# Kernel tuning notes

Hardware: AMD Instinct MI355X
Metric: run time of the kernel (lower is better)

The kernel has to match this reference:

```python
import jax, jax.numpy as jnp
import numpy as np

B, T, C, H = 4, 2048, 1024, 16
DH = C // H  # 64


def setup_inputs() -> dict:
    key = jax.random.key(0)
    k_x, k_qkv, k_proj = jax.random.split(key, 3)
    x = jax.random.normal(k_x, (B, T, C), dtype=jnp.float32)
    # variance-scaling (fan_in) init for linear weights, torch layout [out, in]
    qkv_w = jax.random.normal(k_qkv, (3 * C, C), dtype=jnp.float32) * (1.0 / np.sqrt(C))
    qkv_b = jnp.zeros((3 * C,), dtype=jnp.float32)
    proj_w = jax.random.normal(k_proj, (C, C), dtype=jnp.float32) * (1.0 / np.sqrt(C))
    proj_b = jnp.zeros((C,), dtype=jnp.float32)
    # causal mask, broadcastable to [B, H, T, T]
    mask = jnp.tril(jnp.ones((T, T), dtype=bool))[None, None]
    return {"x": x, "qkv_w": qkv_w, "qkv_b": qkv_b,
            "proj_w": proj_w, "proj_b": proj_b, "mask": mask}


def reference(x, qkv_w, qkv_b, proj_w, proj_b, mask):
    b, t, c = x.shape
    scale = DH ** -0.5
    qkv = (x @ qkv_w.T + qkv_b).reshape(b, t, 3, H, DH)
    qkv = jnp.transpose(qkv, (2, 0, 3, 1, 4))  # [3, B, H, T, DH]
    q, k, v = qkv[0], qkv[1], qkv[2]
    attn = jnp.einsum("bhqd,bhkd->bhqk", q, k) * scale  # [B, H, T, T]
    neg = -jnp.finfo(attn.dtype).max
    attn = jnp.where(mask, attn, neg)
    attn = jax.nn.softmax(attn, axis=-1)
    out = jnp.einsum("bhqk,bhkd->bhqd", attn, v)  # [B, H, T, DH]
    out = jnp.transpose(out, (0, 2, 1, 3)).reshape(b, t, c)
    return out @ proj_w.T + proj_b
```

## Files before the change

kernel.cpp:

```cpp
#include <hip/hip_runtime.h>
#include <hip/hip_bf16.h>
#include <stdint.h>

#define B_ 4
#define T_ 2048
#define C_ 1024
#define H_ 16
#define DH_ 64
#define M_ (B_*T_)
#define NQKV_ (3*C_)
#define K_ C_

typedef __attribute__((ext_vector_type(8))) short short8;
typedef __attribute__((ext_vector_type(4))) float f32x4;
typedef __attribute__((ext_vector_type(4))) unsigned short us4;

union BFC { __hip_bfloat16 h; unsigned short u; };
__device__ inline unsigned short f2b(float f){ BFC c; c.h = __float2bfloat16(f); return c.u; }

__device__ inline void gload_lds16(const void* g, void* l){
  __builtin_amdgcn_global_load_lds(
    (const __attribute__((address_space(1))) void*)(uintptr_t)g,
    (__attribute__((address_space(3))) void*)(uintptr_t)l,
    16, 0, 0);
}

__global__ void cvt_f32_bf16(const float* __restrict__ src,
                             __hip_bfloat16* __restrict__ dst, int n4)
{
  int i = blockIdx.x * blockDim.x + threadIdx.x;
  int stride = gridDim.x * blockDim.x;
  for (; i < n4; i += stride) {
    float4 v = reinterpret_cast<const float4*>(src)[i];
    us4 o;
    o.x = f2b(v.x); o.y = f2b(v.y); o.z = f2b(v.z); o.w = f2b(v.w);
    reinterpret_cast<us4*>(dst)[i] = o;
  }
}

__global__ __launch_bounds__(256) void gemm_bt(
    const __hip_bfloat16* __restrict__ A,
    const __hip_bfloat16* __restrict__ Bw,
    const float* __restrict__ bias,
    int mode,
    __hip_bfloat16* __restrict__ qdst,
    __hip_bfloat16* __restrict__ kdst,
    __hip_bfloat16* __restrict__ vdst,
    float* __restrict__ fdst)
{
  __shared__ char a_lds[8192];
  __shared__ char b_lds[8192];

  const int tid = threadIdx.x;
  const int lane = tid & 63;
  const int w = tid >> 6;
  const int l15 = lane & 15;
  const int lhi = lane >> 4;
  const int wm = w >> 1, wn = w & 1;
  const int row0 = blockIdx.y * 128;
  const int col0 = blockIdx.x * 128;

  int srow[2], scol[2];
#pragma unroll
  for (int j = 0; j < 2; ++j) {
    int L = w * 2048 + j * 1024 + lane * 16;
    int r = L >> 6;
    int cb = (L & 63) ^ (((r >> 1) & 3) << 4);
    srow[j] = r;
    scol[j] = cb >> 1;
  }

  const f32x4 zf = {0.f, 0.f, 0.f, 0.f};
  f32x4 acc[4][4];
#pragma unroll
  for (int m = 0; m < 4; ++m)
#pragma unroll
    for (int n = 0; n < 4; ++n) acc[m][n] = zf;

  const short* Ag = (const short*)A;
  const short* Bg = (const short*)Bw;

  for (int kt = 0; kt < K_; kt += 32) {
    gload_lds16(Ag + (size_t)(row0 + srow[0]) * K_ + kt + scol[0], a_lds + w * 2048);
    gload_lds16(Ag + (size_t)(row0 + srow[1]) * K_ + kt + scol[1], a_lds + w * 2048 + 1024);
    gload_lds16(Bg + (size_t)(col0 + srow[0]) * K_ + kt + scol[0], b_lds + w * 2048);
    gload_lds16(Bg + (size_t)(col0 + srow[1]) * K_ + kt + scol[1], b_lds + w * 2048 + 1024);
    __syncthreads();

    short8 af[4], bfr[4];
#pragma unroll
    for (int m = 0; m < 4; ++m) {
      int r = wm * 64 + m * 16 + l15;
      af[m] = *(const short8*)(a_lds + r * 64 + ((lhi * 16) ^ (((r >> 1) & 3) << 4)));
    }
#pragma unroll
    for (int n = 0; n < 4; ++n) {
      int r = wn * 64 + n * 16 + l15;
      bfr[n] = *(const short8*)(b_lds + r * 64 + ((lhi * 16) ^ (((r >> 1) & 3) << 4)));
    }
#pragma unroll
    for (int m = 0; m < 4; ++m)
#pragma unroll
      for (int n = 0; n < 4; ++n)
        acc[m][n] = __builtin_amdgcn_mfma_f32_16x16x32_bf16(af[m], bfr[n], acc[m][n], 0, 0, 0);
    __syncthreads();
  }

  if (mode == 0) {
#pragma unroll
    for (int m = 0; m < 4; ++m) {
#pragma unroll
      for (int r = 0; r < 4; ++r) {
        int grow = row0 + wm * 64 + m * 16 + lhi * 4 + r;
        int b = grow >> 11, tt = grow & 2047;
#pragma unroll
        for (int n = 0; n < 4; ++n) {
          int gcol = col0 + wn * 64 + n * 16 + l15;
          float v = acc[m][n][r] + bias[gcol];
          int sel = gcol >> 10;
          int c1 = gcol & 1023;
          int hh = c1 >> 6, dh = c1 & 63;
          __hip_bfloat16 bv = __float2bfloat16(v);
          if (sel == 0)
            qdst[(((size_t)(b * H_ + hh)) * T_ + tt) * DH_ + dh] = bv;
          else if (sel == 1)
            kdst[(((size_t)(b * H_ + hh)) * T_ + tt) * DH_ + dh] = bv;
          else
            vdst[(((size_t)(b * H_ + hh)) * DH_ + dh) * T_ + tt] = bv;
        }
      }
    }
  } else {
#pragma unroll
    for (int m = 0; m < 4; ++m) {
#pragma unroll
      for (int r = 0; r < 4; ++r) {
        int grow = row0 + wm * 64 + m * 16 + lhi * 4 + r;
#pragma unroll
        for (int n = 0; n < 4; ++n) {
          int gcol = col0 + wn * 64 + n * 16 + l15;
          fdst[(size_t)grow * C_ + gcol] = acc[m][n][r] + bias[gcol];
        }
      }
    }
  }
}

__global__ __launch_bounds__(512, 2) void attn_kernel(
    const __hip_bfloat16* __restrict__ qg,
    const __hip_bfloat16* __restrict__ kg,
    const __hip_bfloat16* __restrict__ vtg,
    __hip_bfloat16* __restrict__ og)
{
  __shared__ char k_lds[2][8192];
  __shared__ char v_lds[2][8192];
  __shared__ char p_lds[8][4096];

  const int tid = threadIdx.x;
  const int lane = tid & 63;
  const int w = tid >> 6;
  const int l15 = lane & 15;
  const int lhi = lane >> 4;
  const int blk = blockIdx.x;
  const int bh = blk & 63;
  const int g = blk >> 6;
  const int qb = (g < 4) ? g : 11 - g;
  const int qr0 = qb * 256 + w * 32;
  const int nt = 4 * (qb + 1);
  const int tmask = qr0 >> 6;

  const char* kpb = (const char*)(kg + (size_t)bh * T_ * DH_);
  const char* vtpb = (const char*)(vtg + (size_t)bh * DH_ * T_);
  const short* qp = (const short*)(qg + (size_t)bh * T_ * DH_);
  char* pwl = p_lds[w];

  const int srow = tid >> 3;
  const int scb = ((tid & 7) << 4) ^ ((srow & 7) << 4);
  const int sdst = tid * 16;

  short8 qf[2][2];
#pragma unroll
  for (int m = 0; m < 2; ++m)
#pragma unroll
    for (int kf = 0; kf < 2; ++kf)
      qf[m][kf] = *(const short8*)(qp + (size_t)(qr0 + m * 16 + l15) * DH_ +
                                   kf * 32 + lhi * 8);

  const f32x4 zf = {0.f, 0.f, 0.f, 0.f};
  f32x4 o[2][4];
  float lsum[2][4];
#pragma unroll
  for (int m = 0; m < 2; ++m) {
#pragma unroll
    for (int n = 0; n < 4; ++n) o[m][n] = zf;
#pragma unroll
    for (int r = 0; r < 4; ++r) lsum[m][r] = 0.f;
  }

  gload_lds16(kpb + (size_t)srow * 128 + scb, &k_lds[0][sdst]);
  gload_lds16(vtpb + (size_t)srow * 4096 + scb, &v_lds[0][sdst]);
  __syncthreads();

  for (int t = 0; t < nt; ++t) {
    const int cur = t & 1;
    if (t + 1 < nt) {
      const int kv1 = (t + 1) * 64;
      gload_lds16(kpb + (size_t)(kv1 + srow) * 128 + scb, &k_lds[cur ^ 1][sdst]);
      gload_lds16(vtpb + (size_t)srow * 4096 + kv1 * 2 + scb, &v_lds[cur ^ 1][sdst]);
    }

    if (t <= tmask) {
      const int kv0 = t * 64;

      short8 kfr[2][4];
#pragma unroll
      for (int kf = 0; kf < 2; ++kf)
#pragma unroll
        for (int n = 0; n < 4; ++n) {
          int kr = n * 16 + l15;
          kfr[kf][n] = *(const short8*)(&k_lds[cur][kr * 128 +
                           ((kf * 64 + lhi * 16) ^ ((kr & 7) << 4))]);
        }

      f32x4 s[2][4];
#pragma unroll
      for (int m = 0; m < 2; ++m)
#pragma unroll
        for (int n = 0; n < 4; ++n) s[m][n] = zf;
#pragma unroll
      for (int kf = 0; kf < 2; ++kf)
#pragma unroll
        for (int n = 0; n < 4; ++n)
#pragma unroll
          for (int m = 0; m < 2; ++m)
            s[m][n] = __builtin_amdgcn_mfma_f32_16x16x32_bf16(qf[m][kf], kfr[kf][n],
                                                              s[m][n], 0, 0, 0);

      short8 vfr[2][4];
#pragma unroll
      for (int kf = 0; kf < 2; ++kf)
#pragma unroll
        for (int n = 0; n < 4; ++n) {
          int vr = n * 16 + l15;
          vfr[kf][n] = *(const short8*)(&v_lds[cur][vr * 128 +
                           ((kf * 64 + lhi * 16) ^ ((vr & 7) << 4))]);
        }

      if (t == tmask) {
#pragma unroll
        for (int m = 0; m < 2; ++m)
#pragma unroll
          for (int n = 0; n < 4; ++n)
#pragma unroll
            for (int r = 0; r < 4; ++r) {
              int kvA = kv0 + n * 16 + l15;
              int qA = qr0 + m * 16 + lhi * 4 + r;
              if (kvA > qA) s[m][n][r] = -1e30f;
            }
      }

#pragma unroll
      for (int m = 0; m < 2; ++m)
#pragma unroll
        for (int n = 0; n < 4; ++n)
#pragma unroll
          for (int r = 0; r < 4; ++r) {
            float pe = __expf(s[m][n][r] * 0.125f);
            s[m][n][r] = pe;
            lsum[m][r] += pe;
          }

#pragma unroll
      for (int m = 0; m < 2; ++m)
#pragma unroll
        for (int n = 0; n < 4; ++n)
#pragma unroll
          for (int r = 0; r < 4; ++r) {
            int row = m * 16 + lhi * 4 + r;
            *(unsigned short*)(pwl + row * 128 +
                               (((n * 16 + l15) * 2) ^ ((row & 7) << 4))) =
                f2b(s[m][n][r]);
          }
      short8 pa[2][2];
#pragma unroll
      for (int m = 0; m < 2; ++m)
#pragma unroll
        for (int kf = 0; kf < 2; ++kf) {
          int row = m * 16 + l15;
          pa[m][kf] = *(const short8*)(pwl + row * 128 +
                                       ((kf * 64 + lhi * 16) ^ ((row & 7) << 4)));
        }

#pragma unroll
      for (int kf = 0; kf < 2; ++kf)
#pragma unroll
        for (int n = 0; n < 4; ++n)
#pragma unroll
          for (int m = 0; m < 2; ++m)
            o[m][n] = __builtin_amdgcn_mfma_f32_16x16x32_bf16(pa[m][kf], vfr[kf][n],
                                                              o[m][n], 0, 0, 0);
    }

    __syncthreads();
  }

#pragma unroll
  for (int m = 0; m < 2; ++m)
#pragma unroll
    for (int r = 0; r < 4; ++r)
#pragma unroll
      for (int d = 1; d < 16; d <<= 1)
        lsum[m][r] += __shfl_xor(lsum[m][r], d, 64);

  const int b = bh >> 4, hd = bh & 15;
#pragma unroll
  for (int m = 0; m < 2; ++m)
#pragma unroll
    for (int r = 0; r < 4; ++r) {
      float inv = 1.f / lsum[m][r];
      int qrow = qr0 + m * 16 + lhi * 4 + r;
      __hip_bfloat16* orow = og + ((size_t)(b * T_ + qrow)) * C_ + hd * DH_;
#pragma unroll
      for (int n = 0; n < 4; ++n)
        orow[n * 16 + l15] = __float2bfloat16(o[m][n][r] * inv);
    }
}

extern "C" void kernel_launch(void* const* d_in, const int* in_sizes, int n_in,
                              void* d_out, int out_size, void* d_ws, size_t ws_size,
                              hipStream_t stream) {
  const float* x      = (const float*)d_in[0];
  const float* qkv_w  = (const float*)d_in[1];
  const float* qkv_b  = (const float*)d_in[2];
  const float* proj_w = (const float*)d_in[3];
  const float* proj_b = (const float*)d_in[4];
  float* out = (float*)d_out;

  char* ws = (char*)d_ws;
  __hip_bfloat16* xb    = (__hip_bfloat16*)(ws);
  __hip_bfloat16* wqkv  = (__hip_bfloat16*)(ws + 16777216);
  __hip_bfloat16* wproj = (__hip_bfloat16*)(ws + 23068672);
  __hip_bfloat16* qb    = (__hip_bfloat16*)(ws + 25165824);
  __hip_bfloat16* kb    = (__hip_bfloat16*)(ws + 41943040);
  __hip_bfloat16* vtb   = (__hip_bfloat16*)(ws + 58720256);
  __hip_bfloat16* att   = (__hip_bfloat16*)(ws + 75497472);

  cvt_f32_bf16<<<2048, 256, 0, stream>>>(x, xb, M_ * K_ / 4);
  cvt_f32_bf16<<<1024, 256, 0, stream>>>(qkv_w, wqkv, NQKV_ * K_ / 4);
  cvt_f32_bf16<<<512, 256, 0, stream>>>(proj_w, wproj, C_ * K_ / 4);

  gemm_bt<<<dim3(NQKV_ / 128, M_ / 128), 256, 0, stream>>>(
      xb, wqkv, qkv_b, 0, qb, kb, vtb, nullptr);

  attn_kernel<<<dim3(512), 512, 0, stream>>>(qb, kb, vtb, att);

  gemm_bt<<<dim3(C_ / 128, M_ / 128), 256, 0, stream>>>(
      att, wproj, proj_b, 1, nullptr, nullptr, nullptr, out);
}
```

Before: 207.7 us.

## Double-buffer GEMM LDS tiles and remap workgroups across XCDs

The bf16 GEMM now uses two LDS buffers, so it issues the next K-tile's global-to-LDS loads before running the MFMAs on the current tile. This is meant to hide global load latency behind compute. It also launches a 1D grid and permutes block IDs so that consecutive logical tiles are grouped per XCD (blockIdx & 7), aiming for better L2 reuse of the A and B panels. The cost is twice the LDS per block, which may lower occupancy, and the remap assumes the grid size is divisible by 8.

```diff
diff --git a/kernel.cpp b/kernel.cpp
--- a/kernel.cpp
+++ b/kernel.cpp
@@ -42,14 +42,14 @@
     const __hip_bfloat16* __restrict__ A,
     const __hip_bfloat16* __restrict__ Bw,
     const float* __restrict__ bias,
-    int mode,
+    int mode, int nbx,
     __hip_bfloat16* __restrict__ qdst,
     __hip_bfloat16* __restrict__ kdst,
     __hip_bfloat16* __restrict__ vdst,
     float* __restrict__ fdst)
 {
-  __shared__ char a_lds[8192];
-  __shared__ char b_lds[8192];
+  __shared__ char a_lds[2][8192];
+  __shared__ char b_lds[2][8192];
 
   const int tid = threadIdx.x;
   const int lane = tid & 63;
@@ -57,8 +57,13 @@
   const int l15 = lane & 15;
   const int lhi = lane >> 4;
   const int wm = w >> 1, wn = w & 1;
-  const int row0 = blockIdx.y * 128;
-  const int col0 = blockIdx.x * 128;
+
+  const int nwg = gridDim.x;
+  const int q8 = nwg >> 3;
+  const int lb = (blockIdx.x & 7) * q8 + (blockIdx.x >> 3);
+  const int bx = lb % nbx, by = lb / nbx;
+  const int row0 = by * 128;
+  const int col0 = bx * 128;
 
   int srow[2], scol[2];
 #pragma unroll
@@ -80,31 +85,48 @@
   const short* Ag = (const short*)A;
   const short* Bg = (const short*)Bw;
 
-  for (int kt = 0; kt < K_; kt += 32) {
-    gload_lds16(Ag + (size_t)(row0 + srow[0]) * K_ + kt + scol[0], a_lds + w * 2048);
-    gload_lds16(Ag + (size_t)(row0 + srow[1]) * K_ + kt + scol[1], a_lds + w * 2048 + 1024);
-    gload_lds16(Bg + (size_t)(col0 + srow[0]) * K_ + kt + scol[0], b_lds + w * 2048);
-    gload_lds16(Bg + (size_t)(col0 + srow[1]) * K_ + kt + scol[1], b_lds + w * 2048 + 1024);
-    __syncthreads();
+#define STAGE(kt, buf)                                                          \
+  do {                                                                          \
+    gload_lds16(Ag + (size_t)(row0 + srow[0]) * K_ + (kt) + scol[0],            \
+                &a_lds[buf][w * 2048]);                                         \
+    gload_lds16(Ag + (size_t)(row0 + srow[1]) * K_ + (kt) + scol[1],            \
+                &a_lds[buf][w * 2048 + 1024]);                                  \
+    gload_lds16(Bg + (size_t)(col0 + srow[0]) * K_ + (kt) + scol[0],            \
+                &b_lds[buf][w * 2048]);                                         \
+    gload_lds16(Bg + (size_t)(col0 + srow[1]) * K_ + (kt) + scol[1],            \
+                &b_lds[buf][w * 2048 + 1024]);                                  \
+  } while (0)
+
+  STAGE(0, 0);
+  __syncthreads();
+
+  const int NKT = K_ / 32;
+  for (int ki = 0; ki < NKT; ++ki) {
+    const int cur = ki & 1;
+    if (ki + 1 < NKT) STAGE((ki + 1) * 32, cur ^ 1);
 
     short8 af[4], bfr[4];
 #pragma unroll
     for (int m = 0; m < 4; ++m) {
       int r = wm * 64 + m * 16 + l15;
-      af[m] = *(const short8*)(a_lds + r * 64 + ((lhi * 16) ^ (((r >> 1) & 3) << 4)));
+      af[m] = *(const short8*)(&a_lds[cur][r * 64 +
+                   ((lhi * 16) ^ (((r >> 1) & 3) << 4))]);
     }
 #pragma unroll
     for (int n = 0; n < 4; ++n) {
       int r = wn * 64 + n * 16 + l15;
-      bfr[n] = *(const short8*)(b_lds + r * 64 + ((lhi * 16) ^ (((r >> 1) & 3) << 4)));
+      bfr[n] = *(const short8*)(&b_lds[cur][r * 64 +
+                   ((lhi * 16) ^ (((r >> 1) & 3) << 4))]);
     }
 #pragma unroll
     for (int m = 0; m < 4; ++m)
 #pragma unroll
       for (int n = 0; n < 4; ++n)
         acc[m][n] = __builtin_amdgcn_mfma_f32_16x16x32_bf16(af[m], bfr[n], acc[m][n], 0, 0, 0);
+
     __syncthreads();
   }
+#undef STAGE
 
   if (mode == 0) {
 #pragma unroll
@@ -349,11 +371,11 @@
   cvt_f32_bf16<<<1024, 256, 0, stream>>>(qkv_w, wqkv, NQKV_ * K_ / 4);
   cvt_f32_bf16<<<512, 256, 0, stream>>>(proj_w, wproj, C_ * K_ / 4);
 
-  gemm_bt<<<dim3(NQKV_ / 128, M_ / 128), 256, 0, stream>>>(
-      xb, wqkv, qkv_b, 0, qb, kb, vtb, nullptr);
+  gemm_bt<<<dim3((NQKV_/128) * (M_/128)), 256, 0, stream>>>(
+      xb, wqkv, qkv_b, 0, NQKV_/128, qb, kb, vtb, nullptr);
 
   attn_kernel<<<dim3(512), 512, 0, stream>>>(qb, kb, vtb, att);
 
-  gemm_bt<<<dim3(C_ / 128, M_ / 128), 256, 0, stream>>>(
-      att, wproj, proj_b, 1, nullptr, nullptr, nullptr, out);
-}
+  gemm_bt<<<dim3((C_/128) * (M_/128)), 256, 0, stream>>>(
+      att, wproj, proj_b, 1, C_/128, nullptr, nullptr, nullptr, out);
+}
```

After: 208.8 us. Within noise of the previous version (+0.6%).
